# Performance work log

Measured on AMD Instinct MI355X. Metric: run time of the kernel, lower is better.

Reference implementation:

```python
import jax, jax.numpy as jnp
import numpy as np

NUM_GRAPHS = 512   # number of graphs in the batch
MAX_NODES = 192    # static pad bound (actual sizes are in [96,160])
TOTAL = 65536      # total atoms across all graphs
D = 256            # model dim (from MultiheadAttention(256, 4))
H = 4              # heads
DH = D // H        # head dim = 64


def setup_inputs() -> dict:
    # Ragged graph sizes that sum exactly to TOTAL (pairs 128+p / 128-p).
    rng = np.random.default_rng(0)
    p = rng.integers(0, 33, size=NUM_GRAPHS // 2)
    sizes = np.concatenate([128 + p, 128 - p])
    rng.shuffle(sizes)
    batch = np.repeat(np.arange(NUM_GRAPHS, dtype=np.int32), sizes)

    key = jax.random.key(0)
    ks = jax.random.split(key, 12)
    s = 0.02
    return {
        "x": jax.random.normal(ks[0], (TOTAL, D), jnp.float32),
        "batch": jnp.asarray(batch),
        # attn1 (torch MultiheadAttention packed in_proj + out_proj)
        "in_w1": jax.random.normal(ks[1], (3 * D, D), jnp.float32) * s,
        "in_b1": jnp.zeros((3 * D,), jnp.float32),
        "out_w1": jax.random.normal(ks[2], (D, D), jnp.float32) * s,
        "out_b1": jnp.zeros((D,), jnp.float32),
        # attn2
        "in_w2": jax.random.normal(ks[3], (3 * D, D), jnp.float32) * s,
        "in_b2": jnp.zeros((3 * D,), jnp.float32),
        "out_w2": jax.random.normal(ks[4], (D, D), jnp.float32) * s,
        "out_b2": jnp.zeros((D,), jnp.float32),
        # readout MLP: 256 -> 256 -> 128 -> 1 (dropout is identity in eval)
        "r_w1": jax.random.normal(ks[5], (256, 256), jnp.float32) * s,
        "r_b1": jnp.zeros((256,), jnp.float32),
        "r_w2": jax.random.normal(ks[6], (128, 256), jnp.float32) * s,
        "r_b2": jnp.zeros((128,), jnp.float32),
        "r_w3": jax.random.normal(ks[7], (1, 128), jnp.float32) * s,
        "r_b3": jnp.zeros((1,), jnp.float32),
    }


def _mha(xd, mask, in_w, in_b, out_w, out_b):
    # xd: [B, L, D], mask: [B, L] (True = valid key). torch MHA semantics.
    B, L, _ = xd.shape
    qkv = xd @ in_w.T + in_b                                  # [B, L, 3D]
    q, k, v = jnp.split(qkv, 3, axis=-1)
    split = lambda t: t.reshape(B, L, H, DH).transpose(0, 2, 1, 3)  # [B,H,L,DH]
    q, k, v = split(q), split(k), split(v)
    scores = jnp.einsum("bhqd,bhkd->bhqk", q, k) / jnp.sqrt(jnp.float32(DH))
    scores = jnp.where(mask[:, None, None, :], scores, -jnp.inf)
    attn = jax.nn.softmax(scores, axis=-1)                    # each graph has >=1 node
    o = jnp.einsum("bhqk,bhkd->bhqd", attn, v)                # [B,H,L,DH]
    o = o.transpose(0, 2, 1, 3).reshape(B, L, D)
    return o @ out_w.T + out_b


def reference(x, batch, in_w1, in_b1, out_w1, out_b1,
              in_w2, in_b2, out_w2, out_b2,
              r_w1, r_b1, r_w2, r_b2, r_w3, r_b3):
    # Scatter ragged atoms into a padded dense [B, MAX_NODES, D] block
    # (equivalent to the per-graph Python loop, but one fused pass).
    idx = jnp.arange(TOTAL)
    pos = idx - jnp.searchsorted(batch, batch, side="left")   # position within graph
    dense = jnp.zeros((NUM_GRAPHS, MAX_NODES, D), x.dtype).at[batch, pos].set(x)
    mask = jnp.zeros((NUM_GRAPHS, MAX_NODES), bool).at[batch, pos].set(True)

    h = _mha(dense, mask, in_w1, in_b1, out_w1, out_b1)
    h = _mha(h, mask, in_w2, in_b2, out_w2, out_b2)

    # masked mean-pool over valid nodes of each graph
    m = mask[..., None].astype(h.dtype)
    pooled = (h * m).sum(axis=1) / m.sum(axis=1)              # [B, D]

    h1 = jax.nn.relu(pooled @ r_w1.T + r_b1)                  # dropout = identity (eval)
    h2 = jax.nn.relu(h1 @ r_w2.T + r_b2)
    energy = h2 @ r_w3.T + r_b3                               # [B, 1]
    return energy[:, 0]                                       # (batch_size,)
```

## Files before the change

### kernel.cpp

```cpp
#include <hip/hip_runtime.h>
#include <math.h>

#define TOTAL 65536
#define NG 512
#define DMODEL 256
#define QKVLD 768

typedef __attribute__((ext_vector_type(8))) short bf16x8;
typedef __attribute__((ext_vector_type(4))) float f32x4;

__device__ inline ushort f2bf(float f) {
    unsigned int u = __float_as_uint(f);
    unsigned int r = (u + 0x7FFFu + ((u >> 16) & 1u)) >> 16;
    return (ushort)r;
}
__device__ inline float bf2f(ushort h) { return __uint_as_float(((unsigned int)h) << 16); }

__device__ __forceinline__ void llds16(const void* gptr, void* lptr) {
    __builtin_amdgcn_global_load_lds(
        (const __attribute__((address_space(1))) unsigned int*)gptr,
        (__attribute__((address_space(3))) unsigned int*)lptr, 16, 0, 0);
}

__global__ __launch_bounds__(256) void prep_kernel(
    const float* __restrict__ x, const float* __restrict__ in_w1,
    const float* __restrict__ in_w2, const float* __restrict__ out_w1,
    const float* __restrict__ out_b1, const float* __restrict__ in_b2,
    const int* __restrict__ batch,
    ushort* __restrict__ xb, ushort* __restrict__ Wb1,
    ushort* __restrict__ Wc2b, float* __restrict__ bc2, int* __restrict__ starts)
{
    const int b = blockIdx.x, t = threadIdx.x;
    if (b < 16384) {
        int i = b * 256 + t;
        float4 v = ((const float4*)x)[i];
        ushort4 u;
        u.x = f2bf(v.x); u.y = f2bf(v.y); u.z = f2bf(v.z); u.w = f2bf(v.w);
        ((ushort4*)xb)[i] = u;
    } else if (b < 16576) {
        int i = (b - 16384) * 256 + t;
        float4 v = ((const float4*)in_w1)[i];
        ushort4 u;
        u.x = f2bf(v.x); u.y = f2bf(v.y); u.z = f2bf(v.z); u.w = f2bf(v.w);
        ((ushort4*)Wb1)[i] = u;
    } else if (b < 17344) {
        const int n = b - 16576;
        __shared__ float wrow[256];
        wrow[t] = in_w2[n * 256 + t];
        __syncthreads();
        float s = 0.f;
#pragma unroll 8
        for (int j = 0; j < 256; ++j) s += wrow[j] * out_w1[j * 256 + t];
        Wc2b[n * 256 + t] = f2bf(s);
    } else if (b < 17347) {
        int n = (b - 17344) * 256 + t;
        if (n < 768) {
            float s = 0.f;
            for (int j = 0; j < 256; ++j) s += in_w2[n * 256 + j] * out_b1[j];
            bc2[n] = s + in_b2[n];
        }
    } else {
        int g = (b - 17347) * 256 + t;
        if (g < NG) {
            int lo = 0, hi = TOTAL;
            while (lo < hi) {
                int mid = (lo + hi) >> 1;
                if (batch[mid] < g) lo = mid + 1; else hi = mid;
            }
            starts[g] = lo;
            if (g == 0) starts[NG] = TOTAL;
        }
    }
}

__global__ __launch_bounds__(256) void gemm_mfma(
    const ushort* __restrict__ A,
    const ushort* __restrict__ W,
    const float* __restrict__ bias,
    ushort* __restrict__ C, int ldc)
{
    __shared__ ushort As[128 * 64];
    __shared__ ushort Bs[128 * 64];
    const int tid = threadIdx.x;
    const int lane = tid & 63, wid = tid >> 6;
    const int grp = lane >> 4, ln16 = lane & 15;
    const int wm = wid & 1, wn = wid >> 1;

    const int bid = blockIdx.x;
    const int xcd = bid & 7;
    const int j6  = bid >> 3;
    const int mt  = xcd * 64 + j6 / 6;
    const int nt  = j6 % 6;
    const int n0 = nt * 128, m0 = mt * 128;

    const int lrow = lane >> 3;
    const int lchunk = (lane & 7) ^ lrow;

    f32x4 acc[4][4];
#pragma unroll
    for (int i = 0; i < 4; ++i)
#pragma unroll
        for (int j = 0; j < 4; ++j) acc[i][j] = (f32x4){0.f, 0.f, 0.f, 0.f};

    for (int k0 = 0; k0 < 256; k0 += 64) {
#pragma unroll
        for (int j = 0; j < 4; ++j) {
            int band = wid * 32 + j * 8;
            int row = band + lrow;
            llds16(A + (size_t)(m0 + row) * 256 + k0 + lchunk * 8, &As[band * 64]);
            llds16(W + (size_t)(n0 + row) * 256 + k0 + lchunk * 8, &Bs[band * 64]);
        }
        __syncthreads();
#pragma unroll
        for (int kc = 0; kc < 2; ++kc) {
            bf16x8 a[4], b[4];
#pragma unroll
            for (int i = 0; i < 4; ++i) {
                int r = wm * 64 + i * 16 + ln16;
                int p = (kc * 4 + grp) ^ (r & 7);
                a[i] = *(const bf16x8*)&As[r * 64 + p * 8];
            }
#pragma unroll
            for (int j = 0; j < 4; ++j) {
                int r = wn * 64 + j * 16 + ln16;
                int p = (kc * 4 + grp) ^ (r & 7);
                b[j] = *(const bf16x8*)&Bs[r * 64 + p * 8];
            }
#pragma unroll
            for (int i = 0; i < 4; ++i)
#pragma unroll
                for (int j = 0; j < 4; ++j)
                    acc[i][j] = __builtin_amdgcn_mfma_f32_16x16x32_bf16(a[i], b[j], acc[i][j], 0, 0, 0);
        }
        __syncthreads();
    }

#pragma unroll
    for (int j = 0; j < 4; ++j) {
        int col = n0 + wn * 64 + j * 16 + ln16;
        float bv = bias[col];
#pragma unroll
        for (int i = 0; i < 4; ++i) {
            int r0 = m0 + wm * 64 + i * 16 + grp * 4;
#pragma unroll
            for (int reg = 0; reg < 4; ++reg)
                C[(size_t)(r0 + reg) * ldc + col] = f2bf(acc[i][j][reg] + bv);
        }
    }
}

#define VLD 168
#define PLD 40

__global__ __launch_bounds__(512) void attn_mfma(const ushort* __restrict__ qkv,
                                                 ushort* __restrict__ obuf,
                                                 float* __restrict__ psumOut,
                                                 const int* __restrict__ starts) {
    __shared__ ushort Ks[160 * 64];
    __shared__ ushort Vt[64 * VLD];
    __shared__ ushort Ps[8 * 16 * PLD];
    __shared__ float  red[8][64];
    const int bid = blockIdx.x;
    const int xcd = bid & 7;
    const int j6  = bid >> 3;
    const int g = xcd * 64 + (j6 & 63);
    const int h = j6 >> 6;
    int s = starts[g];
    int e = starts[g + 1];
    s = (s < 0) ? 0 : ((s > TOTAL) ? TOTAL : s);
    e = (e < s) ? s : ((e > TOTAL) ? TOTAL : e);
    int L = e - s;
    if (L > 160) L = 160;
    if (L < 1) L = 1;
    const int ktL = (L + 15) >> 4;
    const int tid = threadIdx.x;
    const int lane = tid & 63, wid = tid >> 6;
    const int grp = lane >> 4, ln16 = lane & 15;
    const int lrow = lane >> 3;
    const int lchunk = (lane & 7) ^ lrow;

#pragma unroll
    for (int r = 0; r < 3; ++r) {
        int bi = r * 8 + wid;
        if (bi < 20) {
            int band = bi * 8;
            int row = band + lrow;
            int crow = (row < L) ? row : (L - 1);
            llds16(qkv + (size_t)(s + crow) * QKVLD + 256 + h * 64 + lchunk * 8, &Ks[band * 64]);
        }
    }
#pragma unroll
    for (int r = 0; r < 3; ++r) {
        int idx = r * 512 + tid;
        if (idx < 1280) {
            int kc = idx >> 6;
            int d = idx & 63;
            ushort tmp[8];
#pragma unroll
            for (int j = 0; j < 8; ++j) {
                int key = kc * 8 + j;
                int ckey = (key < L) ? key : (L - 1);
                tmp[j] = qkv[(size_t)(s + ckey) * QKVLD + 512 + h * 64 + d];
            }
            *(uint4*)&Vt[d * VLD + kc * 8] = *(const uint4*)tmp;
        }
    }
    __syncthreads();

    ushort* myP = &Ps[wid * 16 * PLD];
    float psum[4] = {0.f, 0.f, 0.f, 0.f};
    const bool pooled = (psumOut != nullptr);

    for (int q0 = wid * 16; q0 < L; q0 += 128) {
        bf16x8 qa[2];
        {
            int qi = q0 + ln16;
            int grow = (qi < L) ? (s + qi) : s;
            const ushort* qbase = qkv + (size_t)grow * QKVLD + h * 64;
            qa[0] = *(const bf16x8*)(qbase + grp * 8);
            qa[1] = *(const bf16x8*)(qbase + 32 + grp * 8);
        }
        f32x4 sc[10];
#pragma unroll
        for (int kt = 0; kt < 10; ++kt) {
            if (kt < ktL) {
                int row = kt * 16 + ln16;
                int p0 = grp ^ (row & 7);
                int p1 = (4 + grp) ^ (row & 7);
                bf16x8 b0 = *(const bf16x8*)&Ks[row * 64 + p0 * 8];
                bf16x8 b1 = *(const bf16x8*)&Ks[row * 64 + p1 * 8];
                f32x4 z = (f32x4){0.f, 0.f, 0.f, 0.f};
                z = __builtin_amdgcn_mfma_f32_16x16x32_bf16(qa[0], b0, z, 0, 0, 0);
                z = __builtin_amdgcn_mfma_f32_16x16x32_bf16(qa[1], b1, z, 0, 0, 0);
                sc[kt] = z;
            }
        }
        float sm[4] = {0.f, 0.f, 0.f, 0.f};
#pragma unroll
        for (int kt = 0; kt < 10; ++kt) {
            if (kt < ktL) {
                bool dead = (kt * 16 + ln16) >= L;
#pragma unroll
                for (int r = 0; r < 4; ++r) {
                    float p = __expf(dead ? -INFINITY : sc[kt][r] * 0.125f);
                    sc[kt][r] = p;
                    sm[r] += p;
                }
            } else {
#pragma unroll
                for (int r = 0; r < 4; ++r) sc[kt][r] = 0.f;
            }
        }
#pragma unroll
        for (int m = 1; m <= 8; m <<= 1)
#pragma unroll
            for (int r = 0; r < 4; ++r) sm[r] += __shfl_xor(sm[r], m, 64);
        float inv[4];
#pragma unroll
        for (int r = 0; r < 4; ++r) inv[r] = 1.f / sm[r];

        f32x4 o[4];
#pragma unroll
        for (int dt = 0; dt < 4; ++dt) o[dt] = (f32x4){0.f, 0.f, 0.f, 0.f};
#pragma unroll
        for (int st = 0; st < 5; ++st) {
            if (st * 32 < L) {
#pragma unroll
                for (int kti = 0; kti < 2; ++kti) {
                    int kt = st * 2 + kti;
#pragma unroll
                    for (int r = 0; r < 4; ++r)
                        myP[(grp * 4 + r) * PLD + kti * 16 + ln16] = f2bf(sc[kt][r]);
                }
                bf16x8 pa = *(const bf16x8*)&myP[ln16 * PLD + grp * 8];
#pragma unroll
                for (int dt = 0; dt < 4; ++dt) {
                    bf16x8 vb = *(const bf16x8*)&Vt[(dt * 16 + ln16) * VLD + st * 32 + grp * 8];
                    o[dt] = __builtin_amdgcn_mfma_f32_16x16x32_bf16(pa, vb, o[dt], 0, 0, 0);
                }
            }
        }
        if (pooled) {
#pragma unroll
            for (int dt = 0; dt < 4; ++dt)
#pragma unroll
                for (int reg = 0; reg < 4; ++reg) {
                    int q = q0 + grp * 4 + reg;
                    if (q < L) psum[dt] += o[dt][reg] * inv[reg];
                }
        } else {
#pragma unroll
            for (int dt = 0; dt < 4; ++dt)
#pragma unroll
                for (int reg = 0; reg < 4; ++reg) {
                    int q = q0 + grp * 4 + reg;
                    if (q < L)
                        obuf[(size_t)(s + q) * DMODEL + h * 64 + dt * 16 + ln16] =
                            f2bf(o[dt][reg] * inv[reg]);
                }
        }
    }

    if (pooled) {
#pragma unroll
        for (int dt = 0; dt < 4; ++dt) {
            psum[dt] += __shfl_xor(psum[dt], 16, 64);
            psum[dt] += __shfl_xor(psum[dt], 32, 64);
        }
        if (grp == 0) {
#pragma unroll
            for (int dt = 0; dt < 4; ++dt) red[wid][dt * 16 + ln16] = psum[dt];
        }
        __syncthreads();
        if (tid < 64) {
            float v = 0.f;
#pragma unroll
            for (int w = 0; w < 8; ++w) v += red[w][tid];
            psumOut[g * DMODEL + h * 64 + tid] = v;
        }
    }
}

__global__ __launch_bounds__(256) void readout_kernel(
    const float* __restrict__ psum, const int* __restrict__ starts,
    const float* __restrict__ ow2, const float* __restrict__ ob2,
    const float* __restrict__ w1, const float* __restrict__ b1,
    const float* __restrict__ w2, const float* __restrict__ b2,
    const float* __restrict__ w3, const float* __restrict__ b3,
    float* __restrict__ out)
{
    __shared__ float xs[256], ps[256], h1s[256], h2s[128];
    const int g = blockIdx.x, t = threadIdx.x;
    int s = starts[g], e = starts[g + 1];
    s = (s < 0) ? 0 : ((s > TOTAL) ? TOTAL : s);
    e = (e < s) ? s : ((e > TOTAL) ? TOTAL : e);
    int L = e - s;
    if (L < 1) L = 1;
    xs[t] = psum[g * 256 + t] / (float)L;
    __syncthreads();
    {
        const float* wr = ow2 + t * 256;
        float s0 = 0.f;
#pragma unroll 8
        for (int i = 0; i < 256; ++i) s0 += xs[i] * wr[i];
        ps[t] = s0 + ob2[t];
    }
    __syncthreads();
    {
        const float* wr = w1 + t * 256;
        float s0 = 0.f;
#pragma unroll 8
        for (int i = 0; i < 256; ++i) s0 += ps[i] * wr[i];
        float v = s0 + b1[t];
        h1s[t] = v > 0.f ? v : 0.f;
    }
    __syncthreads();
    if (t < 128) {
        const float* wr = w2 + t * 256;
        float s0 = 0.f;
#pragma unroll 8
        for (int i = 0; i < 256; ++i) s0 += h1s[i] * wr[i];
        float v = s0 + b2[t];
        h2s[t] = v > 0.f ? v : 0.f;
    }
    __syncthreads();
    if (t < 64) {
        float v = h2s[t] * w3[t] + h2s[t + 64] * w3[t + 64];
#pragma unroll
        for (int off = 32; off > 0; off >>= 1) v += __shfl_down(v, off, 64);
        if (t == 0) out[g] = v + b3[0];
    }
}

__global__ __launch_bounds__(256) void zero_out_kernel(float* __restrict__ out, int n) {
    int i = blockIdx.x * 256 + threadIdx.x;
    if (i < n) out[i] = 0.f;
}

extern "C" void kernel_launch(void* const* d_in, const int* in_sizes, int n_in,
                              void* d_out, int out_size, void* d_ws, size_t ws_size,
                              hipStream_t stream) {
    float* out = (float*)d_out;

    const int expect[16] = {
        TOTAL * DMODEL, TOTAL,
        3 * DMODEL * DMODEL, 3 * DMODEL,
        DMODEL * DMODEL, DMODEL,
        3 * DMODEL * DMODEL, 3 * DMODEL,
        DMODEL * DMODEL, DMODEL,
        256 * 256, 256,
        128 * 256, 128,
        128, 1
    };
    const size_t NEEDED = 135536640ull;
    bool ok = (n_in == 16) && (out_size == NG) && (d_ws != nullptr) && (ws_size >= NEEDED);
    if (ok) {
        for (int i = 0; i < 16; ++i)
            if (in_sizes[i] != expect[i]) { ok = false; break; }
    }
    if (!ok) {
        zero_out_kernel<<<(out_size + 255) / 256, 256, 0, stream>>>(out, out_size);
        return;
    }

    const float* x      = (const float*)d_in[0];
    const int*   batch  = (const int*)d_in[1];
    const float* in_w1  = (const float*)d_in[2];
    const float* in_b1  = (const float*)d_in[3];
    const float* out_w1 = (const float*)d_in[4];
    const float* out_b1 = (const float*)d_in[5];
    const float* in_w2  = (const float*)d_in[6];
    const float* in_b2  = (const float*)d_in[7];
    const float* out_w2 = (const float*)d_in[8];
    const float* out_b2 = (const float*)d_in[9];
    const float* r_w1   = (const float*)d_in[10];
    const float* r_b1   = (const float*)d_in[11];
    const float* r_w2   = (const float*)d_in[12];
    const float* r_b2   = (const float*)d_in[13];
    const float* r_w3   = (const float*)d_in[14];
    const float* r_b3   = (const float*)d_in[15];

    char* ws = (char*)d_ws;
    int*    starts = (int*)(ws + 0);
    float*  bc2    = (float*)(ws + 4096);
    float*  psum   = (float*)(ws + 8192);
    ushort* Wc2b   = (ushort*)(ws + 532480);
    ushort* Wb1    = (ushort*)(ws + 925696);
    ushort* bufO   = (ushort*)(ws + 1318912);
    ushort* bufQKV = (ushort*)(ws + 34873344ull);

    prep_kernel<<<17349, 256, 0, stream>>>(x, in_w1, in_w2, out_w1, out_b1, in_b2,
                                           batch, bufO, Wb1, Wc2b, bc2, starts);

    gemm_mfma<<<3072, 256, 0, stream>>>(bufO, Wb1, in_b1, bufQKV, QKVLD);
    attn_mfma<<<2048, 512, 0, stream>>>(bufQKV, bufO, nullptr, starts);

    gemm_mfma<<<3072, 256, 0, stream>>>(bufO, Wc2b, bc2, bufQKV, QKVLD);
    attn_mfma<<<2048, 512, 0, stream>>>(bufQKV, bufO, psum, starts);

    readout_kernel<<<NG, 256, 0, stream>>>(psum, starts, out_w2, out_b2,
                                           r_w1, r_b1, r_w2, r_b2, r_w3, r_b3, out);
}
```

Before: 332.6 us.

## Fold softmax scale into Q, use exp2 and hardware bf16 convert, coalesce readout

The QKV GEMM epilogue now pre-multiplies Q columns by log2(e)/sqrt(dh), so the attention softmax can use a raw exp2 with no per-score multiply. Software bf16 rounding is replaced by the hardware v_cvt_pk_bf16_f32 instruction in several stores. The readout MLP is restructured so 16 lanes cooperatively read each weight row as float4 and reduce with shuffles, which gives coalesced weight loads instead of strided per-thread row reads. The scaling changes rounding slightly because Q is scaled before it is cast to bf16.

```diff
diff --git a/kernel.cpp b/kernel.cpp
--- a/kernel.cpp
+++ b/kernel.cpp
@@ -14,7 +14,14 @@
     unsigned int r = (u + 0x7FFFu + ((u >> 16) & 1u)) >> 16;
     return (ushort)r;
 }
+__device__ __forceinline__ ushort f2bf_hw(float f) {
+    unsigned int r;
+    asm("v_cvt_pk_bf16_f32 %0, %1, %2" : "=v"(r) : "v"(f), "v"(0.f));
+    return (ushort)r;
+}
 __device__ inline float bf2f(ushort h) { return __uint_as_float(((unsigned int)h) << 16); }
+
+#define QSCALE 0.18033688011112042f
 
 __device__ __forceinline__ void llds16(const void* gptr, void* lptr) {
     __builtin_amdgcn_global_load_lds(
@@ -135,6 +142,7 @@
         __syncthreads();
     }
 
+    const float cs = (n0 < 256) ? QSCALE : 1.0f;
 #pragma unroll
     for (int j = 0; j < 4; ++j) {
         int col = n0 + wn * 64 + j * 16 + ln16;
@@ -144,7 +152,7 @@
             int r0 = m0 + wm * 64 + i * 16 + grp * 4;
 #pragma unroll
             for (int reg = 0; reg < 4; ++reg)
-                C[(size_t)(r0 + reg) * ldc + col] = f2bf(acc[i][j][reg] + bv);
+                C[(size_t)(r0 + reg) * ldc + col] = f2bf_hw((acc[i][j][reg] + bv) * cs);
         }
     }
 }
@@ -242,7 +250,8 @@
                 bool dead = (kt * 16 + ln16) >= L;
 #pragma unroll
                 for (int r = 0; r < 4; ++r) {
-                    float p = __expf(dead ? -INFINITY : sc[kt][r] * 0.125f);
+                    float p = __builtin_amdgcn_exp2f(sc[kt][r]);
+                    p = dead ? 0.f : p;
                     sc[kt][r] = p;
                     sm[r] += p;
                 }
@@ -270,7 +279,7 @@
                     int kt = st * 2 + kti;
 #pragma unroll
                     for (int r = 0; r < 4; ++r)
-                        myP[(grp * 4 + r) * PLD + kti * 16 + ln16] = f2bf(sc[kt][r]);
+                        myP[(grp * 4 + r) * PLD + kti * 16 + ln16] = f2bf_hw(sc[kt][r]);
                 }
                 bf16x8 pa = *(const bf16x8*)&myP[ln16 * PLD + grp * 8];
 #pragma unroll
@@ -296,7 +305,7 @@
                     int q = q0 + grp * 4 + reg;
                     if (q < L)
                         obuf[(size_t)(s + q) * DMODEL + h * 64 + dt * 16 + ln16] =
-                            f2bf(o[dt][reg] * inv[reg]);
+                            f2bf_hw(o[dt][reg] * inv[reg]);
                 }
         }
     }
@@ -329,46 +338,86 @@
     const float* __restrict__ w3, const float* __restrict__ b3,
     float* __restrict__ out)
 {
-    __shared__ float xs[256], ps[256], h1s[256], h2s[128];
+    __shared__ __attribute__((aligned(16))) float xs[256];
+    __shared__ __attribute__((aligned(16))) float ps[256];
+    __shared__ __attribute__((aligned(16))) float h1s[256];
+    __shared__ __attribute__((aligned(16))) float h2s[128];
     const int g = blockIdx.x, t = threadIdx.x;
-    int s = starts[g], e = starts[g + 1];
-    s = (s < 0) ? 0 : ((s > TOTAL) ? TOTAL : s);
-    e = (e < s) ? s : ((e > TOTAL) ? TOTAL : e);
-    int L = e - s;
-    if (L < 1) L = 1;
-    xs[t] = psum[g * 256 + t] / (float)L;
+    const int lane = t & 63, wid = t >> 6;
+    const int l16 = lane & 15, gq = lane >> 4;
+
+    {
+        int s = starts[g], e = starts[g + 1];
+        s = (s < 0) ? 0 : ((s > TOTAL) ? TOTAL : s);
+        e = (e < s) ? s : ((e > TOTAL) ? TOTAL : e);
+        int L = e - s;
+        if (L < 1) L = 1;
+        xs[t] = psum[g * 256 + t] / (float)L;
+    }
     __syncthreads();
-    {
-        const float* wr = ow2 + t * 256;
-        float s0 = 0.f;
-#pragma unroll 8
-        for (int i = 0; i < 256; ++i) s0 += xs[i] * wr[i];
-        ps[t] = s0 + ob2[t];
+
+#pragma unroll 4
+    for (int o = 0; o < 16; ++o) {
+        int tt = wid * 64 + o * 4 + gq;
+        const float4* wrow = (const float4*)(ow2 + tt * 256);
+        float a = 0.f;
+#pragma unroll
+        for (int k = 0; k < 4; ++k) {
+            float4 wv = wrow[l16 + k * 16];
+            float4 xv = ((const float4*)xs)[l16 + k * 16];
+            a += wv.x * xv.x + wv.y * xv.y + wv.z * xv.z + wv.w * xv.w;
+        }
+#pragma unroll
+        for (int m = 1; m <= 8; m <<= 1) a += __shfl_xor(a, m, 64);
+        if (l16 == 0) ps[tt] = a + ob2[tt];
     }
     __syncthreads();
-    {
-        const float* wr = w1 + t * 256;
-        float s0 = 0.f;
-#pragma unroll 8
-        for (int i = 0; i < 256; ++i) s0 += ps[i] * wr[i];
-        float v = s0 + b1[t];
-        h1s[t] = v > 0.f ? v : 0.f;
+
+#pragma unroll 4
+    for (int o = 0; o < 16; ++o) {
+        int tt = wid * 64 + o * 4 + gq;
+        const float4* wrow = (const float4*)(w1 + tt * 256);
+        float a = 0.f;
+#pragma unroll
+        for (int k = 0; k < 4; ++k) {
+            float4 wv = wrow[l16 + k * 16];
+            float4 xv = ((const float4*)ps)[l16 + k * 16];
+            a += wv.x * xv.x + wv.y * xv.y + wv.z * xv.z + wv.w * xv.w;
+        }
+#pragma unroll
+        for (int m = 1; m <= 8; m <<= 1) a += __shfl_xor(a, m, 64);
+        if (l16 == 0) {
+            float v = a + b1[tt];
+            h1s[tt] = v > 0.f ? v : 0.f;
+        }
     }
     __syncthreads();
-    if (t < 128) {
-        const float* wr = w2 + t * 256;
-        float s0 = 0.f;
-#pragma unroll 8
-        for (int i = 0; i < 256; ++i) s0 += h1s[i] * wr[i];
-        float v = s0 + b2[t];
-        h2s[t] = v > 0.f ? v : 0.f;
+
+#pragma unroll 4
+    for (int o = 0; o < 8; ++o) {
+        int tt = wid * 32 + o * 4 + gq;
+        const float4* wrow = (const float4*)(w2 + tt * 256);
+        float a = 0.f;
+#pragma unroll
+        for (int k = 0; k < 4; ++k) {
+            float4 wv = wrow[l16 + k * 16];
+            float4 xv = ((const float4*)h1s)[l16 + k * 16];
+            a += wv.x * xv.x + wv.y * xv.y + wv.z * xv.z + wv.w * xv.w;
+        }
+#pragma unroll
+        for (int m = 1; m <= 8; m <<= 1) a += __shfl_xor(a, m, 64);
+        if (l16 == 0) {
+            float v = a + b2[tt];
+            h2s[tt] = v > 0.f ? v : 0.f;
+        }
     }
     __syncthreads();
-    if (t < 64) {
-        float v = h2s[t] * w3[t] + h2s[t + 64] * w3[t + 64];
-#pragma unroll
-        for (int off = 32; off > 0; off >>= 1) v += __shfl_down(v, off, 64);
-        if (t == 0) out[g] = v + b3[0];
+
+    if (wid == 0) {
+        float v = h2s[lane] * w3[lane] + h2s[lane + 64] * w3[lane + 64];
+#pragma unroll
+        for (int m = 1; m <= 32; m <<= 1) v += __shfl_xor(v, m, 64);
+        if (lane == 0) out[g] = v + b3[0];
     }
 }
 
```

Result: faster. 312.2 us (-6.1%).
